# Kernel optimization log

Hardware: AMD Instinct MI355X
Metric: run time of the kernel (lower is better)

The kernel has to match this reference:

```python
import jax, jax.numpy as jnp
import numpy as np


def _rot_mat(thetas, scales):
    # thetas, scales: [bs, g] -> [bs, g, 9, 9] bilinear-interpolation matrices
    bs, g = thetas.shape
    t = thetas.reshape(-1)
    s = scales.reshape(-1)
    x = jnp.cos(t) * s
    y = jnp.sin(t) * s
    yp = -y
    z = jnp.zeros_like(x)
    o = jnp.ones_like(x)
    a = x - y; b = x * y; c = x + y; d = a * c; e = a + c
    ap = x - yp; bp = x * yp; cp = x + yp; dp = ap * cp; ep = ap + cp

    def M(rows):
        # rows: 9 lists of 9 [N]-arrays -> [9, 9, N]
        return jnp.stack([jnp.stack(r, axis=0) for r in rows], axis=0)

    ctr = [z, z, z, z, o, z, z, z, z]

    pb1 = M([
        [a, 1 - a, z, z, z, z, z, z, z],
        [z, 1 - y, y, z, z, z, z, z, z],
        [z, z, a, z, z, 1 - a, z, z, z],
        [y, z, z, 1 - y, z, z, z, z, z],
        ctr,
        [z, z, z, z, z, 1 - y, z, z, y],
        [z, z, z, 1 - a, z, z, a, z, z],
        [z, z, z, z, z, z, y, 1 - y, z],
        [z, z, z, z, z, z, z, 1 - a, a]])
    pb2 = M([
        [a, 1 - a, z, z, z, z, z, z, z],
        [z, x - b, b, z, 1 - c + b, y - b, z, z, z],
        [z, z, a, z, z, 1 - a, z, z, z],
        [b, y - b, z, x - b, 1 - c + b, z, z, z, z],
        ctr,
        [z, z, z, z, 1 - c + b, x - b, z, y - b, b],
        [z, z, z, 1 - a, z, z, a, z, z],
        [z, z, z, y - b, 1 - c + b, z, b, x - b, z],
        [z, z, z, z, z, z, z, 1 - a, a]])
    ps1 = M([
        [d, a - d, z, c - d, 1 - e + d, z, z, z, z],
        [z, x - b, b, z, 1 - c + b, y - b, z, z, z],
        [z, c - d, d, z, 1 - e + d, a - d, z, z, z],
        [b, y - b, z, x - b, 1 - c + b, z, z, z, z],
        ctr,
        [z, z, z, z, 1 - c + b, x - b, z, y - b, b],
        [z, z, z, a - d, 1 - e + d, z, d, c - d, z],
        [z, z, z, y - b, 1 - c + b, z, b, x - b, z],
        [z, z, z, z, 1 - e + d, c - d, z, a - d, d]])
    ps2 = pb2  # identical in the source
    nb1 = M([
        [cp, z, z, 1 - cp, z, z, z, z, z],
        [yp, 1 - yp, z, z, z, z, z, z, z],
        [z, 1 - cp, cp, z, z, z, z, z, z],
        [z, z, z, 1 - yp, z, z, yp, z, z],
        ctr,
        [z, z, yp, z, z, 1 - yp, z, z, z],
        [z, z, z, z, z, z, cp, 1 - cp, z],
        [z, z, z, z, z, z, z, 1 - yp, yp],
        [z, z, z, z, z, 1 - cp, z, z, cp]])
    nb2 = M([
        [cp, z, z, 1 - cp, z, z, z, z, z],
        [bp, x - bp, z, yp - bp, 1 - cp + bp, z, z, z, z],
        [z, 1 - cp, cp, z, z, z, z, z, z],
        [z, z, z, x - bp, 1 - cp + bp, z, bp, yp - bp, z],
        ctr,
        [z, yp - bp, bp, z, 1 - cp + bp, x - bp, z, z, z],
        [z, z, z, z, z, z, cp, 1 - cp, z],
        [z, z, z, z, 1 - cp + bp, yp - bp, z, x - bp, bp],
        [z, z, z, z, z, 1 - cp, z, z, cp]])
    ns1 = M([
        [dp, cp - dp, z, ap - dp, 1 - ep + dp, z, z, z, z],
        [bp, x - bp, z, yp - bp, 1 - cp + bp, z, z, z, z],
        [z, ap - dp, dp, z, 1 - ep + dp, cp - dp, z, z, z],
        [z, yp - bp, bp, z, 1 - cp + bp, x - bp, z, z, z],
        ctr,
        [z, z, z, x - bp, 1 - cp + bp, z, bp, yp - bp, z],
        [z, z, z, cp - dp, 1 - ep + dp, z, dp, ap - dp, z],
        [z, z, z, z, 1 - cp + bp, yp - bp, z, x - bp, bp],
        [z, z, z, z, 1 - ep + dp, ap - dp, z, cp - dp, dp]])
    ns2 = nb2  # mirrors the positive branch where small_2 == big_2

    m_pos = (t >= 0.0)[None, None, :]
    m_big = (s >= 1.0)[None, None, :]
    m_1 = (jnp.abs(t) <= jnp.pi / 4)[None, None, :]
    pos = jnp.where(m_big, jnp.where(m_1, pb1, pb2), jnp.where(m_1, ps1, ps2))
    neg = jnp.where(m_big, jnp.where(m_1, nb1, nb2), jnp.where(m_1, ns1, ns2))
    rot = jnp.where(m_pos, pos, neg)  # [9, 9, bs*g]
    return jnp.transpose(rot, (2, 0, 1)).reshape(bs, g, 9, 9)


def _forward(x, thetas, scales, lambdas, weight):
    # x: [B, Cin, H, W]; weight: [n, Cout, Cin, 3, 3]; thetas/scales/lambdas: [B, n]
    B, Cin, H, W = x.shape
    n, Cout = weight.shape[0], weight.shape[1]
    rot = _rot_mat(thetas, scales) * lambdas[:, :, None, None]  # [B, n, 9, 9]
    w9 = weight.reshape(n, Cout, Cin, 9)
    # per-sample transformed kernel: sum over kernel_number n and source taps j
    w = jnp.einsum('bnij,nocj->bioc', rot, w9)  # [B, 9, Cout, Cin]
    w = jnp.transpose(w, (0, 2, 3, 1)).reshape(B * Cout, Cin, 3, 3)
    xg = x.reshape(1, B * Cin, H, W)
    out = jax.lax.conv_general_dilated(
        xg, w, window_strides=(1, 1), padding=((1, 1), (1, 1)),
        dimension_numbers=('NCHW', 'OIHW', 'NCHW'), feature_group_count=B)
    return out.reshape(B, Cout, H, W)


def setup_inputs() -> dict:
    key = jax.random.key(0)
    ks = jax.random.split(key, 5)
    B, Cin, Cout, H, W, n = 16, 256, 256, 64, 64, 4
    x = jax.random.normal(ks[0], (B, Cin, H, W), dtype=jnp.float32)
    thetas = jax.random.uniform(ks[1], (B, n), minval=-1.2, maxval=1.2, dtype=jnp.float32)
    scales = jax.random.uniform(ks[2], (B, n), minval=0.5, maxval=1.5, dtype=jnp.float32)
    lambdas = jax.nn.softmax(jax.random.normal(ks[3], (B, n), dtype=jnp.float32), axis=-1)
    weight = jax.random.normal(ks[4], (n, Cout, Cin, 3, 3), dtype=jnp.float32) * 0.05
    return {"x": x, "thetas": thetas, "scales": scales, "lambdas": lambdas, "weight": weight}


def reference(x, thetas, scales, lambdas, weight):
    return _forward(x, thetas, scales, lambdas, weight)
```

## Files before the change

kernel.cpp:

```cpp
#include <hip/hip_runtime.h>
#include <cstdint>
#include <cstddef>

typedef unsigned short ushort_t;
typedef __attribute__((ext_vector_type(4))) float f32x4;
typedef __attribute__((ext_vector_type(8))) short s16x8;

#define PI_4F 0.78539816339744830962f

__device__ inline ushort_t f2bf(float f) {
  unsigned int u = __float_as_uint(f);
  u = u + 0x7fffu + ((u >> 16) & 1u);
  return (ushort_t)(u >> 16);
}

__global__ void rot_kernel(const float* __restrict__ thetas, const float* __restrict__ scales,
                           const float* __restrict__ lambdas, float* __restrict__ rot) {
  int tid = threadIdx.x;
  float t = thetas[tid], s = scales[tid], lam = lambdas[tid];
  float xv = cosf(t) * s, yv = sinf(t) * s;
  bool pos = (t >= 0.0f), big = (s >= 1.0f), m1 = (fabsf(t) <= PI_4F);
  float M[81];
#pragma unroll
  for (int i = 0; i < 81; ++i) M[i] = 0.0f;
  M[36 + 4] = 1.0f;
  if (pos) {
    float a = xv - yv, bb = xv * yv, c = xv + yv;
    if (m1 && big) {
      M[0] = a; M[1] = 1 - a;
      M[9 + 1] = 1 - yv; M[9 + 2] = yv;
      M[18 + 2] = a; M[18 + 5] = 1 - a;
      M[27 + 0] = yv; M[27 + 3] = 1 - yv;
      M[45 + 5] = 1 - yv; M[45 + 8] = yv;
      M[54 + 3] = 1 - a; M[54 + 6] = a;
      M[63 + 6] = yv; M[63 + 7] = 1 - yv;
      M[72 + 7] = 1 - a; M[72 + 8] = a;
    } else if (m1) {
      float d = a * c, e = a + c;
      M[0] = d; M[1] = a - d; M[3] = c - d; M[4] = 1 - e + d;
      M[9 + 1] = xv - bb; M[9 + 2] = bb; M[9 + 4] = 1 - c + bb; M[9 + 5] = yv - bb;
      M[18 + 1] = c - d; M[18 + 2] = d; M[18 + 4] = 1 - e + d; M[18 + 5] = a - d;
      M[27 + 0] = bb; M[27 + 1] = yv - bb; M[27 + 3] = xv - bb; M[27 + 4] = 1 - c + bb;
      M[45 + 4] = 1 - c + bb; M[45 + 5] = xv - bb; M[45 + 7] = yv - bb; M[45 + 8] = bb;
      M[54 + 3] = a - d; M[54 + 4] = 1 - e + d; M[54 + 6] = d; M[54 + 7] = c - d;
      M[63 + 3] = yv - bb; M[63 + 4] = 1 - c + bb; M[63 + 6] = bb; M[63 + 7] = xv - bb;
      M[72 + 4] = 1 - e + d; M[72 + 5] = c - d; M[72 + 7] = a - d; M[72 + 8] = d;
    } else {
      M[0] = a; M[1] = 1 - a;
      M[9 + 1] = xv - bb; M[9 + 2] = bb; M[9 + 4] = 1 - c + bb; M[9 + 5] = yv - bb;
      M[18 + 2] = a; M[18 + 5] = 1 - a;
      M[27 + 0] = bb; M[27 + 1] = yv - bb; M[27 + 3] = xv - bb; M[27 + 4] = 1 - c + bb;
      M[45 + 4] = 1 - c + bb; M[45 + 5] = xv - bb; M[45 + 7] = yv - bb; M[45 + 8] = bb;
      M[54 + 3] = 1 - a; M[54 + 6] = a;
      M[63 + 3] = yv - bb; M[63 + 4] = 1 - c + bb; M[63 + 6] = bb; M[63 + 7] = xv - bb;
      M[72 + 7] = 1 - a; M[72 + 8] = a;
    }
  } else {
    float yp = -yv;
    float ap = xv - yp, bp = xv * yp, cp = xv + yp;
    if (m1 && big) {
      M[0] = cp; M[3] = 1 - cp;
      M[9 + 0] = yp; M[9 + 1] = 1 - yp;
      M[18 + 1] = 1 - cp; M[18 + 2] = cp;
      M[27 + 3] = 1 - yp; M[27 + 6] = yp;
      M[45 + 2] = yp; M[45 + 5] = 1 - yp;
      M[54 + 6] = cp; M[54 + 7] = 1 - cp;
      M[63 + 7] = 1 - yp; M[63 + 8] = yp;
      M[72 + 5] = 1 - cp; M[72 + 8] = cp;
    } else if (m1) {
      float dp = ap * cp, ep = ap + cp;
      M[0] = dp; M[1] = cp - dp; M[3] = ap - dp; M[4] = 1 - ep + dp;
      M[9 + 0] = bp; M[9 + 1] = xv - bp; M[9 + 3] = yp - bp; M[9 + 4] = 1 - cp + bp;
      M[18 + 1] = ap - dp; M[18 + 2] = dp; M[18 + 4] = 1 - ep + dp; M[18 + 5] = cp - dp;
      M[27 + 1] = yp - bp; M[27 + 2] = bp; M[27 + 4] = 1 - cp + bp; M[27 + 5] = xv - bp;
      M[45 + 3] = xv - bp; M[45 + 4] = 1 - cp + bp; M[45 + 6] = bp; M[45 + 7] = yp - bp;
      M[54 + 3] = cp - dp; M[54 + 4] = 1 - ep + dp; M[54 + 6] = dp; M[54 + 7] = ap - dp;
      M[63 + 4] = 1 - cp + bp; M[63 + 5] = yp - bp; M[63 + 7] = xv - bp; M[63 + 8] = bp;
      M[72 + 4] = 1 - ep + dp; M[72 + 5] = ap - dp; M[72 + 7] = cp - dp; M[72 + 8] = dp;
    } else {
      M[0] = cp; M[3] = 1 - cp;
      M[9 + 0] = bp; M[9 + 1] = xv - bp; M[9 + 3] = yp - bp; M[9 + 4] = 1 - cp + bp;
      M[18 + 1] = 1 - cp; M[18 + 2] = cp;
      M[27 + 3] = xv - bp; M[27 + 4] = 1 - cp + bp; M[27 + 6] = bp; M[27 + 7] = yp - bp;
      M[45 + 1] = yp - bp; M[45 + 2] = bp; M[45 + 4] = 1 - cp + bp; M[45 + 5] = xv - bp;
      M[54 + 6] = cp; M[54 + 7] = 1 - cp;
      M[63 + 4] = 1 - cp + bp; M[63 + 5] = yp - bp; M[63 + 7] = xv - bp; M[63 + 8] = bp;
      M[72 + 5] = 1 - cp; M[72 + 8] = cp;
    }
  }
  float* r = rot + tid * 81;
#pragma unroll
  for (int i = 0; i < 81; ++i) r[i] = M[i] * lam;
}

__global__ void wt_kernel(const float* __restrict__ weight, const float* __restrict__ rot,
                          ushort_t* __restrict__ wtout) {
  const int o = blockIdx.x, bg = blockIdx.y;
  const int c = threadIdx.x;
  float wv[4][9];
#pragma unroll
  for (int n = 0; n < 4; ++n) {
    const float* wp = weight + (((size_t)(n * 256 + o)) * 256 + c) * 9;
#pragma unroll
    for (int j = 0; j < 9; ++j) wv[n][j] = wp[j];
  }
#pragma unroll
  for (int bl = 0; bl < 4; ++bl) {
    const int b = bg * 4 + bl;
#pragma unroll
    for (int i = 0; i < 9; ++i) {
      float acc = 0.0f;
#pragma unroll
      for (int n = 0; n < 4; ++n) {
        const float* r = rot + (b * 4 + n) * 81 + i * 9;
#pragma unroll
        for (int j = 0; j < 9; ++j) acc = fmaf(r[j], wv[n][j], acc);
      }
      wtout[((size_t)((b * 9 + i) * 256 + o)) * 256 + c] = f2bf(acc);
    }
  }
}

__global__ void border_zero(ushort_t* __restrict__ xpad) {
  const int p = blockIdx.x, b = blockIdx.y;
  int h, w;
  if (p < 66) { h = 0; w = p; }
  else if (p < 132) { h = 65; w = p - 66; }
  else if (p < 196) { w = 0; h = p - 131; }
  else { w = 65; h = p - 195; }
  size_t base = ((size_t)(b * 4356 + h * 66 + w)) * 256 + threadIdx.x * 4;
  *(uint2*)(xpad + base) = make_uint2(0u, 0u);
}

__global__ void transpose_kernel(const float* __restrict__ x, ushort_t* __restrict__ xpad) {
  __shared__ ushort_t tile[64][65];
  const int b = blockIdx.z, ct = blockIdx.y, st = blockIdx.x;
  const int t = threadIdx.x;
  const int l = t & 63, wv = t >> 6;
  const int c0 = ct * 64;
  const float* xb = x + ((size_t)(b * 256 + c0)) * 4096 + st * 64;
#pragma unroll
  for (int k = 0; k < 16; ++k) {
    int c_l = wv + 4 * k;
    tile[l][c_l] = f2bf(xb[(size_t)c_l * 4096 + l]);
  }
  __syncthreads();
  const int hw_l0 = t >> 4, c4 = (t & 15) * 4;
#pragma unroll
  for (int k = 0; k < 4; ++k) {
    int w = hw_l0 + 16 * k;
    uint2 v = *(const uint2*)&tile[w][c4];
    *(uint2*)&xpad[((size_t)(b * 4356 + (st + 1) * 66 + (w + 1))) * 256 + c0 + c4] = v;
  }
}

__device__ inline void gload16(const ushort_t* g, ushort_t* l) {
  __builtin_amdgcn_global_load_lds(
      (const __attribute__((address_space(1))) unsigned int*)g,
      (__attribute__((address_space(3))) unsigned int*)l, 16, 0, 0);
}

__global__ __launch_bounds__(256, 2) void conv_kernel(
    const ushort_t* __restrict__ xpad, const ushort_t* __restrict__ wt,
    float* __restrict__ out) {
  __shared__ __align__(16) ushort_t As[3][256 * 32];
  __shared__ __align__(16) ushort_t Bs[3][128 * 32];

  const int id = blockIdx.x;
  const int xcd = id & 7;
  const int j = id >> 3;
  const int b = xcd * 2 + (j >> 5);
  const int ntile = j & 31;

  const int t = threadIdx.x;
  const int wave = t >> 6, lane = t & 63;
  const int wm = wave & 1, wn = wave >> 1;
  const int lr = lane & 15, lq = lane >> 4;
  const int h0 = ntile * 2;

  const ushort_t* wt_b = wt + (size_t)b * 589824;
  const ushort_t* xp_b = xpad + (size_t)b * 1115136;

  const int lrow = t >> 2;
  const int cg8 = (((t & 3) ^ ((t >> 3) & 3)) * 8);

  const int rsw = (lr >> 1) & 3;
  const int aoff = (wm * 128 + lr) * 32 + ((lq ^ rsw) * 8);
  const int boff = (wn * 64 + lr) * 32 + ((lq ^ rsw) * 8);

  f32x4 acc[8][4];
#pragma unroll
  for (int i = 0; i < 8; ++i)
#pragma unroll
    for (int jj = 0; jj < 4; ++jj) acc[i][jj] = (f32x4)(0.0f);

  auto stage = [&](int ks, int buf) {
    const int tap = ks >> 3;
    const int c0k = (ks & 7) << 5;
    const int kh = tap / 3, kw = tap - kh * 3;
    const ushort_t* ga = wt_b + ((size_t)(tap * 256 + lrow)) * 256 + c0k + cg8;
    ushort_t* Ad = &As[buf][wave * 512];
#pragma unroll
    for (int a = 0; a < 4; ++a) gload16(ga + (size_t)a * 64 * 256, Ad + a * 2048);
    const ushort_t* gb = xp_b + ((size_t)((h0 + kh) * 66 + lrow + kw)) * 256 + c0k + cg8;
    ushort_t* Bd = &Bs[buf][wave * 512];
    gload16(gb, Bd);
    gload16(gb + 66 * 256, Bd + 2048);
  };

  auto compute = [&](int buf) {
    const ushort_t* Ab = &As[buf][0];
    const ushort_t* Bb = &Bs[buf][0];
    s16x8 bfr[4];
#pragma unroll
    for (int ni = 0; ni < 4; ++ni)
      bfr[ni] = *(const s16x8*)(Bb + boff + ni * 512);
#pragma unroll
    for (int ms = 0; ms < 8; ++ms) {
      s16x8 af = *(const s16x8*)(Ab + aoff + ms * 512);
#pragma unroll
      for (int ni = 0; ni < 4; ++ni)
        acc[ms][ni] = __builtin_amdgcn_mfma_f32_16x16x32_bf16(af, bfr[ni], acc[ms][ni], 0, 0, 0);
    }
  };

  stage(0, 0);
  stage(1, 1);

  int bc = 0;
  for (int ks = 0; ks < 71; ++ks) {
    asm volatile("s_waitcnt vmcnt(6)" ::: "memory");
    asm volatile("s_barrier" ::: "memory");
    if (ks < 70) {
      int bp = (bc == 0) ? 2 : bc - 1;
      stage(ks + 2, bp);
    }
    compute(bc);
    bc = (bc == 2) ? 0 : bc + 1;
  }
  asm volatile("s_waitcnt vmcnt(0)" ::: "memory");
  asm volatile("s_barrier" ::: "memory");
  compute(bc);

  float* ob = out + ((size_t)(b * 256 + wm * 128)) * 4096 + ntile * 128 + wn * 64 + lr;
#pragma unroll
  for (int ms = 0; ms < 8; ++ms)
#pragma unroll
    for (int r = 0; r < 4; ++r) {
      float* orow = ob + (size_t)(ms * 16 + lq * 4 + r) * 4096;
#pragma unroll
      for (int ni = 0; ni < 4; ++ni) orow[ni * 16] = acc[ms][ni][r];
    }
}

extern "C" void kernel_launch(void* const* d_in, const int* in_sizes, int n_in,
                              void* d_out, int out_size, void* d_ws, size_t ws_size,
                              hipStream_t stream) {
  const float* x = (const float*)d_in[0];
  const float* thetas = (const float*)d_in[1];
  const float* scales = (const float*)d_in[2];
  const float* lambdas = (const float*)d_in[3];
  const float* weight = (const float*)d_in[4];
  float* out = (float*)d_out;

  float* rot_ws = (float*)d_ws;
  ushort_t* wt_ws = (ushort_t*)((char*)d_ws + 32768);
  ushort_t* xpad_ws = (ushort_t*)((char*)d_ws + 32768 + 18874368);

  rot_kernel<<<1, 64, 0, stream>>>(thetas, scales, lambdas, rot_ws);
  wt_kernel<<<dim3(256, 4), 256, 0, stream>>>(weight, rot_ws, wt_ws);
  border_zero<<<dim3(260, 16), 64, 0, stream>>>(xpad_ws);
  transpose_kernel<<<dim3(64, 4, 16), 256, 0, stream>>>(x, xpad_ws);
  conv_kernel<<<512, 256, 0, stream>>>(xpad_ws, wt_ws, out);
}
```

Measured before the change: 241.4 us.

## Fuse all stages into one persistent kernel with a grid barrier

Merges the rotation, weight-mixing, border-zero, transpose and conv kernels into a single 512-block launch. The blocks synchronise through an atomic grid barrier reset by a memset. Each block now computes its own slice of the prep work, and the conv uses 512 threads with an 8-wave 64x64 split and a shared LDS buffer. This removes launch gaps and the intermediate rot buffer. In exchange it relies on all 512 blocks being co-resident, risks deadlock if occupancy is insufficient, and recomputes the rotation matrices per block.

```diff
diff --git a/kernel.cpp b/kernel.cpp
--- a/kernel.cpp
+++ b/kernel.cpp
@@ -14,167 +14,182 @@
   return (ushort_t)(u >> 16);
 }
 
-__global__ void rot_kernel(const float* __restrict__ thetas, const float* __restrict__ scales,
-                           const float* __restrict__ lambdas, float* __restrict__ rot) {
-  int tid = threadIdx.x;
-  float t = thetas[tid], s = scales[tid], lam = lambdas[tid];
-  float xv = cosf(t) * s, yv = sinf(t) * s;
-  bool pos = (t >= 0.0f), big = (s >= 1.0f), m1 = (fabsf(t) <= PI_4F);
-  float M[81];
-#pragma unroll
-  for (int i = 0; i < 81; ++i) M[i] = 0.0f;
-  M[36 + 4] = 1.0f;
-  if (pos) {
-    float a = xv - yv, bb = xv * yv, c = xv + yv;
-    if (m1 && big) {
-      M[0] = a; M[1] = 1 - a;
-      M[9 + 1] = 1 - yv; M[9 + 2] = yv;
-      M[18 + 2] = a; M[18 + 5] = 1 - a;
-      M[27 + 0] = yv; M[27 + 3] = 1 - yv;
-      M[45 + 5] = 1 - yv; M[45 + 8] = yv;
-      M[54 + 3] = 1 - a; M[54 + 6] = a;
-      M[63 + 6] = yv; M[63 + 7] = 1 - yv;
-      M[72 + 7] = 1 - a; M[72 + 8] = a;
-    } else if (m1) {
-      float d = a * c, e = a + c;
-      M[0] = d; M[1] = a - d; M[3] = c - d; M[4] = 1 - e + d;
-      M[9 + 1] = xv - bb; M[9 + 2] = bb; M[9 + 4] = 1 - c + bb; M[9 + 5] = yv - bb;
-      M[18 + 1] = c - d; M[18 + 2] = d; M[18 + 4] = 1 - e + d; M[18 + 5] = a - d;
-      M[27 + 0] = bb; M[27 + 1] = yv - bb; M[27 + 3] = xv - bb; M[27 + 4] = 1 - c + bb;
-      M[45 + 4] = 1 - c + bb; M[45 + 5] = xv - bb; M[45 + 7] = yv - bb; M[45 + 8] = bb;
-      M[54 + 3] = a - d; M[54 + 4] = 1 - e + d; M[54 + 6] = d; M[54 + 7] = c - d;
-      M[63 + 3] = yv - bb; M[63 + 4] = 1 - c + bb; M[63 + 6] = bb; M[63 + 7] = xv - bb;
-      M[72 + 4] = 1 - e + d; M[72 + 5] = c - d; M[72 + 7] = a - d; M[72 + 8] = d;
-    } else {
-      M[0] = a; M[1] = 1 - a;
-      M[9 + 1] = xv - bb; M[9 + 2] = bb; M[9 + 4] = 1 - c + bb; M[9 + 5] = yv - bb;
-      M[18 + 2] = a; M[18 + 5] = 1 - a;
-      M[27 + 0] = bb; M[27 + 1] = yv - bb; M[27 + 3] = xv - bb; M[27 + 4] = 1 - c + bb;
-      M[45 + 4] = 1 - c + bb; M[45 + 5] = xv - bb; M[45 + 7] = yv - bb; M[45 + 8] = bb;
-      M[54 + 3] = 1 - a; M[54 + 6] = a;
-      M[63 + 3] = yv - bb; M[63 + 4] = 1 - c + bb; M[63 + 6] = bb; M[63 + 7] = xv - bb;
-      M[72 + 7] = 1 - a; M[72 + 8] = a;
-    }
-  } else {
-    float yp = -yv;
-    float ap = xv - yp, bp = xv * yp, cp = xv + yp;
-    if (m1 && big) {
-      M[0] = cp; M[3] = 1 - cp;
-      M[9 + 0] = yp; M[9 + 1] = 1 - yp;
-      M[18 + 1] = 1 - cp; M[18 + 2] = cp;
-      M[27 + 3] = 1 - yp; M[27 + 6] = yp;
-      M[45 + 2] = yp; M[45 + 5] = 1 - yp;
-      M[54 + 6] = cp; M[54 + 7] = 1 - cp;
-      M[63 + 7] = 1 - yp; M[63 + 8] = yp;
-      M[72 + 5] = 1 - cp; M[72 + 8] = cp;
-    } else if (m1) {
-      float dp = ap * cp, ep = ap + cp;
-      M[0] = dp; M[1] = cp - dp; M[3] = ap - dp; M[4] = 1 - ep + dp;
-      M[9 + 0] = bp; M[9 + 1] = xv - bp; M[9 + 3] = yp - bp; M[9 + 4] = 1 - cp + bp;
-      M[18 + 1] = ap - dp; M[18 + 2] = dp; M[18 + 4] = 1 - ep + dp; M[18 + 5] = cp - dp;
-      M[27 + 1] = yp - bp; M[27 + 2] = bp; M[27 + 4] = 1 - cp + bp; M[27 + 5] = xv - bp;
-      M[45 + 3] = xv - bp; M[45 + 4] = 1 - cp + bp; M[45 + 6] = bp; M[45 + 7] = yp - bp;
-      M[54 + 3] = cp - dp; M[54 + 4] = 1 - ep + dp; M[54 + 6] = dp; M[54 + 7] = ap - dp;
-      M[63 + 4] = 1 - cp + bp; M[63 + 5] = yp - bp; M[63 + 7] = xv - bp; M[63 + 8] = bp;
-      M[72 + 4] = 1 - ep + dp; M[72 + 5] = ap - dp; M[72 + 7] = cp - dp; M[72 + 8] = dp;
-    } else {
-      M[0] = cp; M[3] = 1 - cp;
-      M[9 + 0] = bp; M[9 + 1] = xv - bp; M[9 + 3] = yp - bp; M[9 + 4] = 1 - cp + bp;
-      M[18 + 1] = 1 - cp; M[18 + 2] = cp;
-      M[27 + 3] = xv - bp; M[27 + 4] = 1 - cp + bp; M[27 + 6] = bp; M[27 + 7] = yp - bp;
-      M[45 + 1] = yp - bp; M[45 + 2] = bp; M[45 + 4] = 1 - cp + bp; M[45 + 5] = xv - bp;
-      M[54 + 6] = cp; M[54 + 7] = 1 - cp;
-      M[63 + 4] = 1 - cp + bp; M[63 + 5] = yp - bp; M[63 + 7] = xv - bp; M[63 + 8] = bp;
-      M[72 + 5] = 1 - cp; M[72 + 8] = cp;
-    }
-  }
-  float* r = rot + tid * 81;
-#pragma unroll
-  for (int i = 0; i < 81; ++i) r[i] = M[i] * lam;
-}
-
-__global__ void wt_kernel(const float* __restrict__ weight, const float* __restrict__ rot,
-                          ushort_t* __restrict__ wtout) {
-  const int o = blockIdx.x, bg = blockIdx.y;
-  const int c = threadIdx.x;
-  float wv[4][9];
-#pragma unroll
-  for (int n = 0; n < 4; ++n) {
-    const float* wp = weight + (((size_t)(n * 256 + o)) * 256 + c) * 9;
-#pragma unroll
-    for (int j = 0; j < 9; ++j) wv[n][j] = wp[j];
-  }
-#pragma unroll
-  for (int bl = 0; bl < 4; ++bl) {
-    const int b = bg * 4 + bl;
-#pragma unroll
-    for (int i = 0; i < 9; ++i) {
-      float acc = 0.0f;
-#pragma unroll
-      for (int n = 0; n < 4; ++n) {
-        const float* r = rot + (b * 4 + n) * 81 + i * 9;
-#pragma unroll
-        for (int j = 0; j < 9; ++j) acc = fmaf(r[j], wv[n][j], acc);
-      }
-      wtout[((size_t)((b * 9 + i) * 256 + o)) * 256 + c] = f2bf(acc);
-    }
-  }
-}
-
-__global__ void border_zero(ushort_t* __restrict__ xpad) {
-  const int p = blockIdx.x, b = blockIdx.y;
-  int h, w;
-  if (p < 66) { h = 0; w = p; }
-  else if (p < 132) { h = 65; w = p - 66; }
-  else if (p < 196) { w = 0; h = p - 131; }
-  else { w = 65; h = p - 195; }
-  size_t base = ((size_t)(b * 4356 + h * 66 + w)) * 256 + threadIdx.x * 4;
-  *(uint2*)(xpad + base) = make_uint2(0u, 0u);
-}
-
-__global__ void transpose_kernel(const float* __restrict__ x, ushort_t* __restrict__ xpad) {
-  __shared__ ushort_t tile[64][65];
-  const int b = blockIdx.z, ct = blockIdx.y, st = blockIdx.x;
-  const int t = threadIdx.x;
-  const int l = t & 63, wv = t >> 6;
-  const int c0 = ct * 64;
-  const float* xb = x + ((size_t)(b * 256 + c0)) * 4096 + st * 64;
-#pragma unroll
-  for (int k = 0; k < 16; ++k) {
-    int c_l = wv + 4 * k;
-    tile[l][c_l] = f2bf(xb[(size_t)c_l * 4096 + l]);
-  }
-  __syncthreads();
-  const int hw_l0 = t >> 4, c4 = (t & 15) * 4;
-#pragma unroll
-  for (int k = 0; k < 4; ++k) {
-    int w = hw_l0 + 16 * k;
-    uint2 v = *(const uint2*)&tile[w][c4];
-    *(uint2*)&xpad[((size_t)(b * 4356 + (st + 1) * 66 + (w + 1))) * 256 + c0 + c4] = v;
-  }
-}
-
 __device__ inline void gload16(const ushort_t* g, ushort_t* l) {
   __builtin_amdgcn_global_load_lds(
       (const __attribute__((address_space(1))) unsigned int*)g,
       (__attribute__((address_space(3))) unsigned int*)l, 16, 0, 0);
 }
 
-__global__ __launch_bounds__(256, 2) void conv_kernel(
-    const ushort_t* __restrict__ xpad, const ushort_t* __restrict__ wt,
-    float* __restrict__ out) {
-  __shared__ __align__(16) ushort_t As[3][256 * 32];
-  __shared__ __align__(16) ushort_t Bs[3][128 * 32];
+__device__ inline void grid_barrier(unsigned int* bar, unsigned int target) {
+  __threadfence();
+  __syncthreads();
+  if (threadIdx.x == 0) {
+    __hip_atomic_fetch_add(bar, 1u, __ATOMIC_ACQ_REL, __HIP_MEMORY_SCOPE_AGENT);
+    while (__hip_atomic_load(bar, __ATOMIC_ACQUIRE, __HIP_MEMORY_SCOPE_AGENT) < target) {}
+  }
+  __syncthreads();
+  __threadfence();
+}
+
+__global__ __launch_bounds__(512, 4) void mega_kernel(
+    const float* __restrict__ x, const float* __restrict__ thetas,
+    const float* __restrict__ scales, const float* __restrict__ lambdas,
+    const float* __restrict__ weight, float* __restrict__ out,
+    unsigned int* __restrict__ bar, ushort_t* __restrict__ wt,
+    ushort_t* __restrict__ xpad) {
+  __shared__ __align__(16) ushort_t smem[3][12288];
 
   const int id = blockIdx.x;
   const int xcd = id & 7;
-  const int j = id >> 3;
-  const int b = xcd * 2 + (j >> 5);
-  const int ntile = j & 31;
-
+  const int jj = id >> 3;
+  const int b = xcd * 2 + (jj >> 5);
+  const int ntile = jj & 31;
   const int t = threadIdx.x;
+
+  float* ldsrot = (float*)&smem[0][0];
+  if (t < 324) ldsrot[t] = 0.0f;
+  __syncthreads();
+  if (t < 4) {
+    const int gi = b * 4 + t;
+    float th = thetas[gi], s = scales[gi], lam = lambdas[gi];
+    float xv = cosf(th) * s, yv = sinf(th) * s;
+    bool pos = (th >= 0.0f), big = (s >= 1.0f), m1 = (fabsf(th) <= PI_4F);
+    float* R = ldsrot + t * 81;
+    R[40] = lam;
+    if (pos) {
+      float a = xv - yv, bb = xv * yv, cc = xv + yv;
+      if (m1 && big) {
+        R[0]=a*lam; R[1]=(1-a)*lam;
+        R[10]=(1-yv)*lam; R[11]=yv*lam;
+        R[20]=a*lam; R[23]=(1-a)*lam;
+        R[27]=yv*lam; R[30]=(1-yv)*lam;
+        R[50]=(1-yv)*lam; R[53]=yv*lam;
+        R[57]=(1-a)*lam; R[60]=a*lam;
+        R[69]=yv*lam; R[70]=(1-yv)*lam;
+        R[79]=(1-a)*lam; R[80]=a*lam;
+      } else if (m1) {
+        float d = a * cc, e = a + cc;
+        R[0]=d*lam; R[1]=(a-d)*lam; R[3]=(cc-d)*lam; R[4]=(1-e+d)*lam;
+        R[10]=(xv-bb)*lam; R[11]=bb*lam; R[13]=(1-cc+bb)*lam; R[14]=(yv-bb)*lam;
+        R[19]=(cc-d)*lam; R[20]=d*lam; R[22]=(1-e+d)*lam; R[23]=(a-d)*lam;
+        R[27]=bb*lam; R[28]=(yv-bb)*lam; R[30]=(xv-bb)*lam; R[31]=(1-cc+bb)*lam;
+        R[49]=(1-cc+bb)*lam; R[50]=(xv-bb)*lam; R[52]=(yv-bb)*lam; R[53]=bb*lam;
+        R[57]=(a-d)*lam; R[58]=(1-e+d)*lam; R[60]=d*lam; R[61]=(cc-d)*lam;
+        R[66]=(yv-bb)*lam; R[67]=(1-cc+bb)*lam; R[69]=bb*lam; R[70]=(xv-bb)*lam;
+        R[76]=(1-e+d)*lam; R[77]=(cc-d)*lam; R[79]=(a-d)*lam; R[80]=d*lam;
+      } else {
+        R[0]=a*lam; R[1]=(1-a)*lam;
+        R[10]=(xv-bb)*lam; R[11]=bb*lam; R[13]=(1-cc+bb)*lam; R[14]=(yv-bb)*lam;
+        R[20]=a*lam; R[23]=(1-a)*lam;
+        R[27]=bb*lam; R[28]=(yv-bb)*lam; R[30]=(xv-bb)*lam; R[31]=(1-cc+bb)*lam;
+        R[49]=(1-cc+bb)*lam; R[50]=(xv-bb)*lam; R[52]=(yv-bb)*lam; R[53]=bb*lam;
+        R[57]=(1-a)*lam; R[60]=a*lam;
+        R[66]=(yv-bb)*lam; R[67]=(1-cc+bb)*lam; R[69]=bb*lam; R[70]=(xv-bb)*lam;
+        R[79]=(1-a)*lam; R[80]=a*lam;
+      }
+    } else {
+      float yp = -yv;
+      float ap = xv - yp, bp = xv * yp, cp = xv + yp;
+      if (m1 && big) {
+        R[0]=cp*lam; R[3]=(1-cp)*lam;
+        R[9]=yp*lam; R[10]=(1-yp)*lam;
+        R[19]=(1-cp)*lam; R[20]=cp*lam;
+        R[30]=(1-yp)*lam; R[33]=yp*lam;
+        R[47]=yp*lam; R[50]=(1-yp)*lam;
+        R[60]=cp*lam; R[61]=(1-cp)*lam;
+        R[70]=(1-yp)*lam; R[71]=yp*lam;
+        R[77]=(1-cp)*lam; R[80]=cp*lam;
+      } else if (m1) {
+        float dp = ap * cp, ep = ap + cp;
+        R[0]=dp*lam; R[1]=(cp-dp)*lam; R[3]=(ap-dp)*lam; R[4]=(1-ep+dp)*lam;
+        R[9]=bp*lam; R[10]=(xv-bp)*lam; R[12]=(yp-bp)*lam; R[13]=(1-cp+bp)*lam;
+        R[19]=(ap-dp)*lam; R[20]=dp*lam; R[22]=(1-ep+dp)*lam; R[23]=(cp-dp)*lam;
+        R[28]=(yp-bp)*lam; R[29]=bp*lam; R[31]=(1-cp+bp)*lam; R[32]=(xv-bp)*lam;
+        R[48]=(xv-bp)*lam; R[49]=(1-cp+bp)*lam; R[51]=bp*lam; R[52]=(yp-bp)*lam;
+        R[57]=(cp-dp)*lam; R[58]=(1-ep+dp)*lam; R[60]=dp*lam; R[61]=(ap-dp)*lam;
+        R[67]=(1-cp+bp)*lam; R[68]=(yp-bp)*lam; R[70]=(xv-bp)*lam; R[71]=bp*lam;
+        R[76]=(1-ep+dp)*lam; R[77]=(ap-dp)*lam; R[79]=(cp-dp)*lam; R[80]=dp*lam;
+      } else {
+        R[0]=cp*lam; R[3]=(1-cp)*lam;
+        R[9]=bp*lam; R[10]=(xv-bp)*lam; R[12]=(yp-bp)*lam; R[13]=(1-cp+bp)*lam;
+        R[19]=(1-cp)*lam; R[20]=cp*lam;
+        R[30]=(xv-bp)*lam; R[31]=(1-cp+bp)*lam; R[33]=bp*lam; R[34]=(yp-bp)*lam;
+        R[46]=(yp-bp)*lam; R[47]=bp*lam; R[49]=(1-cp+bp)*lam; R[50]=(xv-bp)*lam;
+        R[60]=cp*lam; R[61]=(1-cp)*lam;
+        R[67]=(1-cp+bp)*lam; R[68]=(yp-bp)*lam; R[70]=(xv-bp)*lam; R[71]=bp*lam;
+        R[77]=(1-cp)*lam; R[80]=cp*lam;
+      }
+    }
+  }
+  __syncthreads();
+
+  {
+    const int c = t & 255;
+    const int o_base = ntile * 8 + (t >> 8) * 4;
+    float acc[4][9];
+#pragma unroll
+    for (int oo = 0; oo < 4; ++oo)
+#pragma unroll
+      for (int i = 0; i < 9; ++i) acc[oo][i] = 0.0f;
+#pragma unroll
+    for (int n = 0; n < 4; ++n)
+#pragma unroll
+      for (int j2 = 0; j2 < 9; ++j2) {
+        float wv4[4];
+#pragma unroll
+        for (int oo = 0; oo < 4; ++oo)
+          wv4[oo] = weight[((size_t)((n * 256 + o_base + oo)) * 256 + c) * 9 + j2];
+#pragma unroll
+        for (int i = 0; i < 9; ++i) {
+          float r = ldsrot[n * 81 + i * 9 + j2];
+#pragma unroll
+          for (int oo = 0; oo < 4; ++oo) acc[oo][i] = fmaf(r, wv4[oo], acc[oo][i]);
+        }
+      }
+#pragma unroll
+    for (int oo = 0; oo < 4; ++oo)
+#pragma unroll
+      for (int i = 0; i < 9; ++i)
+        wt[((size_t)((b * 9 + i) * 256 + o_base + oo)) * 256 + c] = f2bf(acc[oo][i]);
+  }
+
+  {
+    ushort_t(*tile)[72] = (ushort_t(*)[72]) & smem[0][0];
+#pragma unroll 1
+    for (int k = 0; k < 8; ++k) {
+      const int tu = ntile * 8 + k;
+      const int st = tu >> 2, ct = tu & 3;
+      const float* xb = x + ((size_t)(b * 256 + ct * 64)) * 4096 + st * 64;
+      __syncthreads();
+#pragma unroll
+      for (int kk = 0; kk < 8; ++kk) {
+        int cL = (t >> 6) + 8 * kk;
+        tile[t & 63][cL] = f2bf(xb[(size_t)cL * 4096 + (t & 63)]);
+      }
+      __syncthreads();
+      const int w2 = t >> 3, c8 = (t & 7) * 8;
+      uint4 v = *(const uint4*)&tile[w2][c8];
+      *(uint4*)&xpad[((size_t)(b * 4356 + (st + 1) * 66 + (w2 + 1))) * 256 + ct * 64 + c8] = v;
+    }
+  }
+
+  if (t < 288) {
+    int p = ntile * 8 + (t >> 5);
+    if (p < 260) {
+      int h, w;
+      if (p < 66) { h = 0; w = p; }
+      else if (p < 132) { h = 65; w = p - 66; }
+      else if (p < 196) { w = 0; h = p - 131; }
+      else { w = 65; h = p - 195; }
+      uint4 z4 = make_uint4(0u, 0u, 0u, 0u);
+      *(uint4*)&xpad[((size_t)(b * 4356 + h * 66 + w)) * 256 + (t & 31) * 8] = z4;
+    }
+  }
+
+  grid_barrier(bar, 512u);
+
   const int wave = t >> 6, lane = t & 63;
-  const int wm = wave & 1, wn = wave >> 1;
+  const int wm = wave & 3, wn = wave >> 2;
   const int lr = lane & 15, lq = lane >> 4;
   const int h0 = ntile * 2;
 
@@ -183,44 +198,43 @@
 
   const int lrow = t >> 2;
   const int cg8 = (((t & 3) ^ ((t >> 3) & 3)) * 8);
-
   const int rsw = (lr >> 1) & 3;
-  const int aoff = (wm * 128 + lr) * 32 + ((lq ^ rsw) * 8);
+  const int aoff = (wm * 64 + lr) * 32 + ((lq ^ rsw) * 8);
   const int boff = (wn * 64 + lr) * 32 + ((lq ^ rsw) * 8);
-
-  f32x4 acc[8][4];
-#pragma unroll
-  for (int i = 0; i < 8; ++i)
-#pragma unroll
-    for (int jj = 0; jj < 4; ++jj) acc[i][jj] = (f32x4)(0.0f);
+  const int nrow2 = 2 * (lrow >> 6);
+
+  f32x4 acc[4][4];
+#pragma unroll
+  for (int i = 0; i < 4; ++i)
+#pragma unroll
+    for (int j2 = 0; j2 < 4; ++j2) acc[i][j2] = (f32x4)(0.0f);
 
   auto stage = [&](int ks, int buf) {
     const int tap = ks >> 3;
     const int c0k = (ks & 7) << 5;
     const int kh = tap / 3, kw = tap - kh * 3;
+    ushort_t* As_s = &smem[buf][0];
+    ushort_t* Bs_s = &smem[buf][8192];
     const ushort_t* ga = wt_b + ((size_t)(tap * 256 + lrow)) * 256 + c0k + cg8;
-    ushort_t* Ad = &As[buf][wave * 512];
-#pragma unroll
-    for (int a = 0; a < 4; ++a) gload16(ga + (size_t)a * 64 * 256, Ad + a * 2048);
-    const ushort_t* gb = xp_b + ((size_t)((h0 + kh) * 66 + lrow + kw)) * 256 + c0k + cg8;
-    ushort_t* Bd = &Bs[buf][wave * 512];
-    gload16(gb, Bd);
-    gload16(gb + 66 * 256, Bd + 2048);
+    gload16(ga, As_s + wave * 512);
+    gload16(ga + 128 * 256, As_s + 4096 + wave * 512);
+    const int sp = (h0 + kh) * 66 + kw + lrow + nrow2;
+    gload16(xp_b + (size_t)sp * 256 + c0k + cg8, Bs_s + wave * 512);
   };
 
   auto compute = [&](int buf) {
-    const ushort_t* Ab = &As[buf][0];
-    const ushort_t* Bb = &Bs[buf][0];
+    const ushort_t* Ab = &smem[buf][0];
+    const ushort_t* Bb = &smem[buf][8192];
     s16x8 bfr[4];
 #pragma unroll
     for (int ni = 0; ni < 4; ++ni)
       bfr[ni] = *(const s16x8*)(Bb + boff + ni * 512);
 #pragma unroll
-    for (int ms = 0; ms < 8; ++ms) {
-      s16x8 af = *(const s16x8*)(Ab + aoff + ms * 512);
+    for (int mi = 0; mi < 4; ++mi) {
+      s16x8 af = *(const s16x8*)(Ab + aoff + mi * 512);
 #pragma unroll
       for (int ni = 0; ni < 4; ++ni)
-        acc[ms][ni] = __builtin_amdgcn_mfma_f32_16x16x32_bf16(af, bfr[ni], acc[ms][ni], 0, 0, 0);
+        acc[mi][ni] = __builtin_amdgcn_mfma_f32_16x16x32_bf16(af, bfr[ni], acc[mi][ni], 0, 0, 0);
     }
   };
 
@@ -229,7 +243,7 @@
 
   int bc = 0;
   for (int ks = 0; ks < 71; ++ks) {
-    asm volatile("s_waitcnt vmcnt(6)" ::: "memory");
+    asm volatile("s_waitcnt vmcnt(3)" ::: "memory");
     asm volatile("s_barrier" ::: "memory");
     if (ks < 70) {
       int bp = (bc == 0) ? 2 : bc - 1;
@@ -242,14 +256,14 @@
   asm volatile("s_barrier" ::: "memory");
   compute(bc);
 
-  float* ob = out + ((size_t)(b * 256 + wm * 128)) * 4096 + ntile * 128 + wn * 64 + lr;
-#pragma unroll
-  for (int ms = 0; ms < 8; ++ms)
+  float* ob = out + ((size_t)(b * 256 + wm * 64)) * 4096 + ntile * 128 + wn * 64 + lr;
+#pragma unroll
+  for (int mi = 0; mi < 4; ++mi)
 #pragma unroll
     for (int r = 0; r < 4; ++r) {
-      float* orow = ob + (size_t)(ms * 16 + lq * 4 + r) * 4096;
-#pragma unroll
-      for (int ni = 0; ni < 4; ++ni) orow[ni * 16] = acc[ms][ni][r];
+      float* orow = ob + (size_t)(mi * 16 + lq * 4 + r) * 4096;
+#pragma unroll
+      for (int ni = 0; ni < 4; ++ni) orow[ni * 16] = acc[mi][ni][r];
     }
 }
 
@@ -263,13 +277,11 @@
   const float* weight = (const float*)d_in[4];
   float* out = (float*)d_out;
 
-  float* rot_ws = (float*)d_ws;
-  ushort_t* wt_ws = (ushort_t*)((char*)d_ws + 32768);
-  ushort_t* xpad_ws = (ushort_t*)((char*)d_ws + 32768 + 18874368);
-
-  rot_kernel<<<1, 64, 0, stream>>>(thetas, scales, lambdas, rot_ws);
-  wt_kernel<<<dim3(256, 4), 256, 0, stream>>>(weight, rot_ws, wt_ws);
-  border_zero<<<dim3(260, 16), 64, 0, stream>>>(xpad_ws);
-  transpose_kernel<<<dim3(64, 4, 16), 256, 0, stream>>>(x, xpad_ws);
-  conv_kernel<<<512, 256, 0, stream>>>(xpad_ws, wt_ws, out);
-}
+  unsigned int* bar = (unsigned int*)d_ws;
+  ushort_t* wt_ws = (ushort_t*)((char*)d_ws + 4096);
+  ushort_t* xpad_ws = (ushort_t*)((char*)d_ws + 4096 + 18874368);
+
+  hipMemsetAsync(bar, 0, 64, stream);
+  mega_kernel<<<512, 512, 0, stream>>>(x, thetas, scales, lambdas, weight, out,
+                                       bar, wt_ws, xpad_ws);
+}
```

Result: slower. 493.5 us (+104.4%).

## Use 8 waves per conv block with smaller per-wave tiles and unrolled triple buffering

Applied to the files above, without the earlier changes.

The conv block now runs 512 threads as a 4x2 wave grid, and each wave computes a 64x64 sub-tile, which halves the accumulator count per wave. The staging loads are redistributed across the extra waves. The K loop is manually unrolled by three with fixed LDS buffer pointers, and the wait also drains lgkmcnt. The aim is more waves in flight for latency hiding and less buffer-index arithmetic, at the cost of fewer MFMAs per LDS fragment load and more barrier participants.

```diff
diff --git a/kernel.cpp b/kernel.cpp
--- a/kernel.cpp
+++ b/kernel.cpp
@@ -160,21 +160,24 @@
       (__attribute__((address_space(3))) unsigned int*)l, 16, 0, 0);
 }
 
-__global__ __launch_bounds__(256, 2) void conv_kernel(
+#define WAITB(N)                                                      \
+  asm volatile("s_waitcnt vmcnt(" #N ") lgkmcnt(0)\n\ts_barrier" ::: "memory")
+
+__global__ __launch_bounds__(512, 4) void conv_kernel(
     const ushort_t* __restrict__ xpad, const ushort_t* __restrict__ wt,
     float* __restrict__ out) {
-  __shared__ __align__(16) ushort_t As[3][256 * 32];
-  __shared__ __align__(16) ushort_t Bs[3][128 * 32];
+  __shared__ __align__(16) ushort_t As0[8192], As1[8192], As2[8192];
+  __shared__ __align__(16) ushort_t Bs0[4096], Bs1[4096], Bs2[4096];
 
   const int id = blockIdx.x;
   const int xcd = id & 7;
-  const int j = id >> 3;
-  const int b = xcd * 2 + (j >> 5);
-  const int ntile = j & 31;
+  const int jj = id >> 3;
+  const int b = xcd * 2 + (jj >> 5);
+  const int ntile = jj & 31;
 
   const int t = threadIdx.x;
   const int wave = t >> 6, lane = t & 63;
-  const int wm = wave & 1, wn = wave >> 1;
+  const int wm = wave & 3, wn = wave >> 2;
   const int lr = lane & 15, lq = lane >> 4;
   const int h0 = ntile * 2;
 
@@ -183,73 +186,74 @@
 
   const int lrow = t >> 2;
   const int cg8 = (((t & 3) ^ ((t >> 3) & 3)) * 8);
-
   const int rsw = (lr >> 1) & 3;
-  const int aoff = (wm * 128 + lr) * 32 + ((lq ^ rsw) * 8);
+  const int aoff = (wm * 64 + lr) * 32 + ((lq ^ rsw) * 8);
   const int boff = (wn * 64 + lr) * 32 + ((lq ^ rsw) * 8);
-
-  f32x4 acc[8][4];
-#pragma unroll
-  for (int i = 0; i < 8; ++i)
-#pragma unroll
-    for (int jj = 0; jj < 4; ++jj) acc[i][jj] = (f32x4)(0.0f);
-
-  auto stage = [&](int ks, int buf) {
+  const int nrow2 = 2 * (lrow >> 6);
+
+  f32x4 acc[4][4];
+#pragma unroll
+  for (int i = 0; i < 4; ++i)
+#pragma unroll
+    for (int j2 = 0; j2 < 4; ++j2) acc[i][j2] = (f32x4)(0.0f);
+
+  auto stage = [&](int ks, ushort_t* Ad, ushort_t* Bd) {
     const int tap = ks >> 3;
     const int c0k = (ks & 7) << 5;
     const int kh = tap / 3, kw = tap - kh * 3;
     const ushort_t* ga = wt_b + ((size_t)(tap * 256 + lrow)) * 256 + c0k + cg8;
-    ushort_t* Ad = &As[buf][wave * 512];
-#pragma unroll
-    for (int a = 0; a < 4; ++a) gload16(ga + (size_t)a * 64 * 256, Ad + a * 2048);
-    const ushort_t* gb = xp_b + ((size_t)((h0 + kh) * 66 + lrow + kw)) * 256 + c0k + cg8;
-    ushort_t* Bd = &Bs[buf][wave * 512];
-    gload16(gb, Bd);
-    gload16(gb + 66 * 256, Bd + 2048);
+    gload16(ga, Ad + wave * 512);
+    gload16(ga + 128 * 256, Ad + 4096 + wave * 512);
+    const int sp = (h0 + kh) * 66 + kw + lrow + nrow2;
+    gload16(xp_b + (size_t)sp * 256 + c0k + cg8, Bd + wave * 512);
   };
 
-  auto compute = [&](int buf) {
-    const ushort_t* Ab = &As[buf][0];
-    const ushort_t* Bb = &Bs[buf][0];
+  auto compute = [&](const ushort_t* Ab, const ushort_t* Bb) {
     s16x8 bfr[4];
 #pragma unroll
     for (int ni = 0; ni < 4; ++ni)
       bfr[ni] = *(const s16x8*)(Bb + boff + ni * 512);
 #pragma unroll
-    for (int ms = 0; ms < 8; ++ms) {
-      s16x8 af = *(const s16x8*)(Ab + aoff + ms * 512);
+    for (int mi = 0; mi < 4; ++mi) {
+      s16x8 af = *(const s16x8*)(Ab + aoff + mi * 512);
 #pragma unroll
       for (int ni = 0; ni < 4; ++ni)
-        acc[ms][ni] = __builtin_amdgcn_mfma_f32_16x16x32_bf16(af, bfr[ni], acc[ms][ni], 0, 0, 0);
+        acc[mi][ni] = __builtin_amdgcn_mfma_f32_16x16x32_bf16(af, bfr[ni], acc[mi][ni], 0, 0, 0);
     }
   };
 
-  stage(0, 0);
-  stage(1, 1);
-
-  int bc = 0;
-  for (int ks = 0; ks < 71; ++ks) {
-    asm volatile("s_waitcnt vmcnt(6)" ::: "memory");
-    asm volatile("s_barrier" ::: "memory");
-    if (ks < 70) {
-      int bp = (bc == 0) ? 2 : bc - 1;
-      stage(ks + 2, bp);
-    }
-    compute(bc);
-    bc = (bc == 2) ? 0 : bc + 1;
-  }
-  asm volatile("s_waitcnt vmcnt(0)" ::: "memory");
-  asm volatile("s_barrier" ::: "memory");
-  compute(bc);
-
-  float* ob = out + ((size_t)(b * 256 + wm * 128)) * 4096 + ntile * 128 + wn * 64 + lr;
-#pragma unroll
-  for (int ms = 0; ms < 8; ++ms)
+  stage(0, As0, Bs0);
+  stage(1, As1, Bs1);
+
+#pragma unroll 1
+  for (int kk = 0; kk < 23; ++kk) {
+    const int ks = kk * 3;
+    WAITB(3);
+    stage(ks + 2, As2, Bs2);
+    compute(As0, Bs0);
+    WAITB(3);
+    stage(ks + 3, As0, Bs0);
+    compute(As1, Bs1);
+    WAITB(3);
+    stage(ks + 4, As1, Bs1);
+    compute(As2, Bs2);
+  }
+  WAITB(3);
+  stage(71, As2, Bs2);
+  compute(As0, Bs0);
+  WAITB(3);
+  compute(As1, Bs1);
+  WAITB(0);
+  compute(As2, Bs2);
+
+  float* ob = out + ((size_t)(b * 256 + wm * 64)) * 4096 + ntile * 128 + wn * 64 + lr;
+#pragma unroll
+  for (int mi = 0; mi < 4; ++mi)
 #pragma unroll
     for (int r = 0; r < 4; ++r) {
-      float* orow = ob + (size_t)(ms * 16 + lq * 4 + r) * 4096;
-#pragma unroll
-      for (int ni = 0; ni < 4; ++ni) orow[ni * 16] = acc[ms][ni][r];
+      float* orow = ob + (size_t)(mi * 16 + lq * 4 + r) * 4096;
+#pragma unroll
+      for (int ni = 0; ni < 4; ++ni) orow[ni * 16] = acc[mi][ni][r];
     }
 }
 
@@ -271,5 +275,5 @@
   wt_kernel<<<dim3(256, 4), 256, 0, stream>>>(weight, rot_ws, wt_ws);
   border_zero<<<dim3(260, 16), 64, 0, stream>>>(xpad_ws);
   transpose_kernel<<<dim3(64, 4, 16), 256, 0, stream>>>(x, xpad_ws);
-  conv_kernel<<<512, 256, 0, stream>>>(xpad_ws, wt_ws, out);
-}
+  conv_kernel<<<512, 512, 0, stream>>>(xpad_ws, wt_ws, out);
+}
```

After: 231.8 us. -4.0%, faster.
